# Kernel tuning notes

Measured on AMD Instinct MI355X. Metric: run time of the kernel, lower is better.

## Reference

```python
import jax, jax.numpy as jnp
import numpy as np

NUM_LAYERS = 3


def setup_inputs() -> dict:
    key = jax.random.key(0)
    k1, k2 = jax.random.split(key)
    N = 200000          # num_users + num_items
    D = 64              # latent_dim
    E = 4000000         # number of directed edges
    edge_index = jax.random.randint(k1, (2, E), 0, N, dtype=jnp.int64)
    emb_weight = 0.1 * jax.random.normal(k2, (N, D), dtype=jnp.float32)  # nn.init.normal_(std=0.1)
    return {"edge_index": edge_index, "emb_weight": emb_weight}


def reference(edge_index, emb_weight):
    N, D = emb_weight.shape
    src, dst = edge_index[0], edge_index[1]
    # gcn_norm (no self loops), as used by LGConv
    deg = jax.ops.segment_sum(jnp.ones_like(src, dtype=emb_weight.dtype), dst, num_segments=N)
    dinv = jnp.where(deg > 0, jax.lax.rsqrt(jnp.maximum(deg, 1.0)), 0.0)
    norm = dinv[src] * dinv[dst]            # [E]
    emb0 = emb_weight
    emb = emb0
    acc = emb0                              # running sum over layer embeddings
    for _ in range(NUM_LAYERS):
        msgs = norm[:, None] * emb[src]     # [E, D] irregular gather
        emb = jax.ops.segment_sum(msgs, dst, num_segments=N)  # scatter-add aggregate
        acc = acc + emb
    out = acc / (NUM_LAYERS + 1)            # mean over stacked layer embeddings
    return (emb0, out)
```

## Files before the change

### kernel.cpp

```cpp
#include <hip/hip_runtime.h>

#define DIM 64
#define BNODE_SHIFT 9
#define BNODE (1 << BNODE_SHIFT)
#define MAXNB 512
#define BIN_CHUNK 8192

__device__ inline float bf2f(unsigned short h) {
    return __uint_as_float(((unsigned int)h) << 16);
}
__device__ inline unsigned int f2bf2(float a, float b) {
    unsigned int ua = __float_as_uint(a);
    unsigned int ub = __float_as_uint(b);
    ua = (ua + 0x7FFFu + ((ua >> 16) & 1u)) >> 16;
    ub = (ub + 0x7FFFu + ((ub >> 16) & 1u)) >> 16;
    return ua | (ub << 16);
}

__global__ void hist_kernel(const int* __restrict__ dst, int* __restrict__ bucket_count,
                            int E, int NB) {
    __shared__ int h[MAXNB];
    const int t = threadIdx.x;
    for (int i = t; i < MAXNB; i += blockDim.x) h[i] = 0;
    __syncthreads();
    const long long beg = (long long)blockIdx.x * BIN_CHUNK;
    for (int j = 0; j < BIN_CHUNK / 256; ++j) {
        long long idx = beg + j * 256 + t;
        if (idx < E) atomicAdd(&h[dst[idx] >> BNODE_SHIFT], 1);
    }
    __syncthreads();
    for (int b = t; b < NB; b += blockDim.x)
        if (h[b]) atomicAdd(&bucket_count[b], h[b]);
}

__global__ void __launch_bounds__(MAXNB) bucket_scan_kernel(
        const int* __restrict__ bucket_count, int* __restrict__ bucket_base,
        int* __restrict__ bucket_cursor, int* __restrict__ row_start,
        int NB, int N, int E) {
    __shared__ int s[MAXNB];
    const int t = threadIdx.x;
    int c = (t < NB) ? bucket_count[t] : 0;
    s[t] = c;
    __syncthreads();
    for (int off = 1; off < MAXNB; off <<= 1) {
        int v = s[t];
        int a = (t >= off) ? s[t - off] : 0;
        __syncthreads();
        s[t] = v + a;
        __syncthreads();
    }
    if (t < NB) {
        int excl = s[t] - c;
        bucket_base[t] = excl;
        bucket_cursor[t] = excl;
    }
    if (t == 0) {
        bucket_base[NB] = s[MAXNB - 1];
        row_start[N] = E;
    }
}

__global__ void bin_kernel(const int* __restrict__ src, const int* __restrict__ dst,
                           int* __restrict__ bucket_cursor, unsigned int* __restrict__ packed,
                           int E, int NB) {
    __shared__ int lhist[MAXNB];
    __shared__ int lbase[MAXNB];
    const int t = threadIdx.x;
    for (int i = t; i < MAXNB; i += blockDim.x) lhist[i] = 0;
    __syncthreads();
    const long long beg = (long long)blockIdx.x * BIN_CHUNK;
    for (int j = 0; j < BIN_CHUNK / 256; ++j) {
        long long idx = beg + j * 256 + t;
        if (idx < E) atomicAdd(&lhist[dst[idx] >> BNODE_SHIFT], 1);
    }
    __syncthreads();
    for (int b = t; b < NB; b += blockDim.x) {
        int c = lhist[b];
        lbase[b] = c ? atomicAdd(&bucket_cursor[b], c) : 0;
    }
    __syncthreads();
    for (int i = t; i < MAXNB; i += blockDim.x) lhist[i] = 0;
    __syncthreads();
    for (int j = 0; j < BIN_CHUNK / 256; ++j) {
        long long idx = beg + j * 256 + t;
        if (idx < E) {
            int d = dst[idx];
            int b = d >> BNODE_SHIFT;
            int lpos = atomicAdd(&lhist[b], 1);
            packed[lbase[b] + lpos] =
                (unsigned int)src[idx] | ((unsigned int)(d & (BNODE - 1)) << 18);
        }
    }
}

__global__ void __launch_bounds__(BNODE) csr_kernel(
        const int* __restrict__ bucket_base, const unsigned int* __restrict__ packed,
        int* __restrict__ csr_src, int* __restrict__ row_start,
        float* __restrict__ dinv, float* __restrict__ rs, float* __restrict__ di2,
        int N) {
    __shared__ int hist[BNODE];
    __shared__ int s[BNODE];
    const int t = threadIdx.x;
    const int b = blockIdx.x;
    const int b0 = bucket_base[b];
    const int cnt = bucket_base[b + 1] - b0;
    hist[t] = 0;
    __syncthreads();
    for (int i = t; i < cnt; i += BNODE)
        atomicAdd(&hist[packed[b0 + i] >> 18], 1);
    __syncthreads();
    s[t] = hist[t];
    __syncthreads();
    for (int off = 1; off < BNODE; off <<= 1) {
        int v = s[t];
        int a = (t >= off) ? s[t - off] : 0;
        __syncthreads();
        s[t] = v + a;
        __syncthreads();
    }
    const int deg = hist[t];
    const int excl = s[t] - deg;
    const int node = (b << BNODE_SHIFT) + t;
    if (node < N) {
        row_start[node] = b0 + excl;
        float fd = (float)deg;
        float di = deg > 0 ? rsqrtf(fd) : 0.0f;
        dinv[node] = di;
        rs[node]   = deg > 0 ? sqrtf(fd) : 0.0f;
        di2[node]  = di * di;
    }
    __syncthreads();
    s[t] = excl;
    __syncthreads();
    for (int i = t; i < cnt; i += BNODE) {
        unsigned int p = packed[b0 + i];
        int lpos = atomicAdd(&s[p >> 18], 1);
        csr_src[b0 + lpos] = (int)(p & 0x3FFFFu);
    }
}

__global__ void conv0_kernel(const float* __restrict__ emb0, const float* __restrict__ dinv,
                             float* __restrict__ out_emb0, unsigned int* __restrict__ S0,
                             int n4) {
    int i = blockIdx.x * blockDim.x + threadIdx.x;
    if (i >= n4) return;
    float4 v = ((const float4*)emb0)[i];
    ((float4*)out_emb0)[i] = v;
    float w = dinv[i >> 4];
    uint2 o;
    o.x = f2bf2(w * v.x, w * v.y);
    o.y = f2bf2(w * v.z, w * v.w);
    ((uint2*)S0)[i] = o;
}

__global__ void gather_kernel(const int* __restrict__ row_start,
                              const int* __restrict__ csr_src,
                              const float* __restrict__ di2,
                              const unsigned int* __restrict__ S_in,
                              unsigned int* __restrict__ S_out,
                              int N) {
    int tid = blockIdx.x * blockDim.x + threadIdx.x;
    int node = tid >> 3;
    int q = tid & 7;
    if (node >= N) return;
    const int beg = row_start[node];
    const int end = row_start[node + 1];
    float r0 = 0.f, r1 = 0.f, r2 = 0.f, r3 = 0.f, r4 = 0.f, r5 = 0.f, r6 = 0.f, r7 = 0.f;
    for (int i = beg; i < end; ++i) {
        int sIdx = csr_src[i];
        uint4 g = *(const uint4*)(S_in + (size_t)sIdx * (DIM / 2) + q * 4);
        r0 += bf2f((unsigned short)(g.x & 0xFFFF));
        r1 += bf2f((unsigned short)(g.x >> 16));
        r2 += bf2f((unsigned short)(g.y & 0xFFFF));
        r3 += bf2f((unsigned short)(g.y >> 16));
        r4 += bf2f((unsigned short)(g.z & 0xFFFF));
        r5 += bf2f((unsigned short)(g.z >> 16));
        r6 += bf2f((unsigned short)(g.w & 0xFFFF));
        r7 += bf2f((unsigned short)(g.w >> 16));
    }
    float w = di2[node];
    uint4 o;
    o.x = f2bf2(w * r0, w * r1);
    o.y = f2bf2(w * r2, w * r3);
    o.z = f2bf2(w * r4, w * r5);
    o.w = f2bf2(w * r6, w * r7);
    *(uint4*)(S_out + (size_t)node * (DIM / 2) + q * 4) = o;
}

__global__ void combine_kernel(const float* __restrict__ emb0, const float* __restrict__ rs,
                               const unsigned int* __restrict__ S1,
                               const unsigned int* __restrict__ S2,
                               const unsigned int* __restrict__ S3,
                               float* __restrict__ acc, int n4) {
    int i = blockIdx.x * blockDim.x + threadIdx.x;
    if (i >= n4) return;
    float4 e = ((const float4*)emb0)[i];
    uint2 a = ((const uint2*)S1)[i];
    uint2 b = ((const uint2*)S2)[i];
    uint2 c = ((const uint2*)S3)[i];
    float w = rs[i >> 4];
    float4 o;
    o.x = 0.25f * (e.x + w * (bf2f(a.x & 0xFFFF) + bf2f(b.x & 0xFFFF) + bf2f(c.x & 0xFFFF)));
    o.y = 0.25f * (e.y + w * (bf2f(a.x >> 16)   + bf2f(b.x >> 16)   + bf2f(c.x >> 16)));
    o.z = 0.25f * (e.z + w * (bf2f(a.y & 0xFFFF) + bf2f(b.y & 0xFFFF) + bf2f(c.y & 0xFFFF)));
    o.w = 0.25f * (e.w + w * (bf2f(a.y >> 16)   + bf2f(b.y >> 16)   + bf2f(c.y >> 16)));
    ((float4*)acc)[i] = o;
}

static inline size_t align256(size_t x) { return (x + 255) & ~(size_t)255; }

extern "C" void kernel_launch(void* const* d_in, const int* in_sizes, int n_in,
                              void* d_out, int out_size, void* d_ws, size_t ws_size,
                              hipStream_t stream) {
    const int*   edge = (const int*)d_in[0];
    const float* emb0 = (const float*)d_in[1];
    const int E = in_sizes[0] / 2;
    const int N = in_sizes[1] / DIM;
    const int* src = edge;
    const int* dst = edge + E;
    const int NB = (N + BNODE - 1) >> BNODE_SHIFT;

    char* ws = (char*)d_ws;
    int* bucket_count  = (int*)ws;  ws += align256((size_t)(MAXNB + 1) * sizeof(int));
    int* bucket_base   = (int*)ws;  ws += align256((size_t)(MAXNB + 1) * sizeof(int));
    int* bucket_cursor = (int*)ws;  ws += align256((size_t)(MAXNB + 1) * sizeof(int));
    int* row_start     = (int*)ws;  ws += align256((size_t)(N + 1) * sizeof(int));
    float* dinv        = (float*)ws; ws += align256((size_t)N * sizeof(float));
    float* rs          = (float*)ws; ws += align256((size_t)N * sizeof(float));
    float* di2         = (float*)ws; ws += align256((size_t)N * sizeof(float));
    unsigned int* packed  = (unsigned int*)ws; ws += align256((size_t)E * sizeof(int));
    int* csr_src       = (int*)ws;  ws += align256((size_t)E * sizeof(int));
    unsigned int* SX   = (unsigned int*)ws; ws += align256((size_t)N * DIM / 2 * sizeof(unsigned int) / 2 * 2 + 256);
    unsigned int* SY   = (unsigned int*)ws; ws += align256((size_t)N * (DIM / 2) * sizeof(unsigned int));
    unsigned int* SZ   = (unsigned int*)ws; ws += align256((size_t)N * (DIM / 2) * sizeof(unsigned int));

    float* out_emb0 = (float*)d_out;
    float* acc      = out_emb0 + (size_t)N * DIM;

    const int blocks_e = (int)(((long long)E + BIN_CHUNK - 1) / BIN_CHUNK);
    const int n4 = N * DIM / 4;

    hipMemsetAsync(bucket_count, 0, (size_t)(MAXNB + 1) * sizeof(int), stream);
    hist_kernel<<<blocks_e, 256, 0, stream>>>(dst, bucket_count, E, NB);
    bucket_scan_kernel<<<1, MAXNB, 0, stream>>>(bucket_count, bucket_base, bucket_cursor,
                                                row_start, NB, N, E);
    bin_kernel<<<blocks_e, 256, 0, stream>>>(src, dst, bucket_cursor, packed, E, NB);
    csr_kernel<<<NB, BNODE, 0, stream>>>(bucket_base, packed, csr_src, row_start,
                                         dinv, rs, di2, N);

    conv0_kernel<<<(n4 + 255) / 256, 256, 0, stream>>>(emb0, dinv, out_emb0, SX, n4);

    const int gthreads = N * 8;
    const int ggrid = (gthreads + 255) / 256;
    gather_kernel<<<ggrid, 256, 0, stream>>>(row_start, csr_src, di2, SX, SY, N);
    gather_kernel<<<ggrid, 256, 0, stream>>>(row_start, csr_src, di2, SY, SX, N);
    gather_kernel<<<ggrid, 256, 0, stream>>>(row_start, csr_src, di2, SX, SZ, N);

    combine_kernel<<<(n4 + 255) / 256, 256, 0, stream>>>(emb0, rs, SY, SX, SZ, acc, n4);
}
```

Measured before the change: 585.6 us.

## Degree-sort nodes per bucket and fuse combine into final gather layer

The CSR kernel now counting-sorts the nodes within each 512-node bucket by degree and emits a per-node descriptor (row begin, row end, node id, 1/deg). The gather kernels walk these descriptors so that neighbouring wavefront lanes handle nodes of similar degree, which is meant to cut loop divergence. The final gather layer folds in the combine step, reading emb0 and the two earlier layer buffers and writing acc directly, which removes a separate pass and the third intermediate buffer. In exchange, the output writes become scattered because nodes are permuted, the CSR kernel gains an extra scan, and the weights are now derived from 1/deg through sqrt and rsqrt.

Measured after the change: 608.1 us. 1.04x slower.

```diff
diff --git a/kernel.cpp b/kernel.cpp
--- a/kernel.cpp
+++ b/kernel.cpp
@@ -6,8 +6,8 @@
 #define MAXNB 512
 #define BIN_CHUNK 8192
 
-__device__ inline float bf2f(unsigned short h) {
-    return __uint_as_float(((unsigned int)h) << 16);
+__device__ inline float bf2f(unsigned int h) {
+    return __uint_as_float((h & 0xFFFFu) << 16);
 }
 __device__ inline unsigned int f2bf2(float a, float b) {
     unsigned int ua = __float_as_uint(a);
@@ -35,8 +35,7 @@
 
 __global__ void __launch_bounds__(MAXNB) bucket_scan_kernel(
         const int* __restrict__ bucket_count, int* __restrict__ bucket_base,
-        int* __restrict__ bucket_cursor, int* __restrict__ row_start,
-        int NB, int N, int E) {
+        int* __restrict__ bucket_cursor, int NB) {
     __shared__ int s[MAXNB];
     const int t = threadIdx.x;
     int c = (t < NB) ? bucket_count[t] : 0;
@@ -54,10 +53,7 @@
         bucket_base[t] = excl;
         bucket_cursor[t] = excl;
     }
-    if (t == 0) {
-        bucket_base[NB] = s[MAXNB - 1];
-        row_start[N] = E;
-    }
+    if (t == 0) bucket_base[NB] = s[MAXNB - 1];
 }
 
 __global__ void bin_kernel(const int* __restrict__ src, const int* __restrict__ dst,
@@ -95,9 +91,8 @@
 
 __global__ void __launch_bounds__(BNODE) csr_kernel(
         const int* __restrict__ bucket_base, const unsigned int* __restrict__ packed,
-        int* __restrict__ csr_src, int* __restrict__ row_start,
-        float* __restrict__ dinv, float* __restrict__ rs, float* __restrict__ di2,
-        int N) {
+        int* __restrict__ csr_src, float* __restrict__ dinv,
+        int4* __restrict__ desc, int N) {
     __shared__ int hist[BNODE];
     __shared__ int s[BNODE];
     const int t = threadIdx.x;
@@ -120,14 +115,13 @@
     }
     const int deg = hist[t];
     const int excl = s[t] - deg;
+    const int myBeg = b0 + excl;
     const int node = (b << BNODE_SHIFT) + t;
+    float di2 = 0.0f;
     if (node < N) {
-        row_start[node] = b0 + excl;
         float fd = (float)deg;
-        float di = deg > 0 ? rsqrtf(fd) : 0.0f;
-        dinv[node] = di;
-        rs[node]   = deg > 0 ? sqrtf(fd) : 0.0f;
-        di2[node]  = di * di;
+        di2 = deg > 0 ? 1.0f / fd : 0.0f;
+        dinv[node] = deg > 0 ? rsqrtf(fd) : 0.0f;
     }
     __syncthreads();
     s[t] = excl;
@@ -137,6 +131,28 @@
         int lpos = atomicAdd(&s[p >> 18], 1);
         csr_src[b0 + lpos] = (int)(p & 0x3FFFFu);
     }
+    __syncthreads();
+    const int bin = deg < (BNODE - 1) ? deg : (BNODE - 1);
+    hist[t] = 0;
+    __syncthreads();
+    atomicAdd(&hist[bin], 1);
+    __syncthreads();
+    s[t] = hist[t];
+    __syncthreads();
+    for (int off = 1; off < BNODE; off <<= 1) {
+        int v = s[t];
+        int a = (t >= off) ? s[t - off] : 0;
+        __syncthreads();
+        s[t] = v + a;
+        __syncthreads();
+    }
+    int tot = hist[t];
+    __syncthreads();
+    hist[t] = s[t] - tot;
+    __syncthreads();
+    int pos = atomicAdd(&hist[bin], 1);
+    desc[(b << BNODE_SHIFT) + pos] =
+        make_int4(myBeg, myBeg + deg, node < N ? node : 0x7FFFFFFF, __float_as_int(di2));
 }
 
 __global__ void conv0_kernel(const float* __restrict__ emb0, const float* __restrict__ dinv,
@@ -153,58 +169,64 @@
     ((uint2*)S0)[i] = o;
 }
 
-__global__ void gather_kernel(const int* __restrict__ row_start,
+template<bool LAST>
+__global__ void gather_kernel(const int4* __restrict__ desc,
                               const int* __restrict__ csr_src,
-                              const float* __restrict__ di2,
                               const unsigned int* __restrict__ S_in,
                               unsigned int* __restrict__ S_out,
-                              int N) {
+                              const unsigned int* __restrict__ S1,
+                              const float* __restrict__ emb0,
+                              float* __restrict__ acc,
+                              int N, int NG) {
     int tid = blockIdx.x * blockDim.x + threadIdx.x;
-    int node = tid >> 3;
+    int g = tid >> 3;
     int q = tid & 7;
+    if (g >= NG) return;
+    const int4 d = desc[g];
+    const int node = d.z;
     if (node >= N) return;
-    const int beg = row_start[node];
-    const int end = row_start[node + 1];
     float r0 = 0.f, r1 = 0.f, r2 = 0.f, r3 = 0.f, r4 = 0.f, r5 = 0.f, r6 = 0.f, r7 = 0.f;
-    for (int i = beg; i < end; ++i) {
+    for (int i = d.x; i < d.y; ++i) {
         int sIdx = csr_src[i];
-        uint4 g = *(const uint4*)(S_in + (size_t)sIdx * (DIM / 2) + q * 4);
-        r0 += bf2f((unsigned short)(g.x & 0xFFFF));
-        r1 += bf2f((unsigned short)(g.x >> 16));
-        r2 += bf2f((unsigned short)(g.y & 0xFFFF));
-        r3 += bf2f((unsigned short)(g.y >> 16));
-        r4 += bf2f((unsigned short)(g.z & 0xFFFF));
-        r5 += bf2f((unsigned short)(g.z >> 16));
-        r6 += bf2f((unsigned short)(g.w & 0xFFFF));
-        r7 += bf2f((unsigned short)(g.w >> 16));
-    }
-    float w = di2[node];
-    uint4 o;
-    o.x = f2bf2(w * r0, w * r1);
-    o.y = f2bf2(w * r2, w * r3);
-    o.z = f2bf2(w * r4, w * r5);
-    o.w = f2bf2(w * r6, w * r7);
-    *(uint4*)(S_out + (size_t)node * (DIM / 2) + q * 4) = o;
-}
-
-__global__ void combine_kernel(const float* __restrict__ emb0, const float* __restrict__ rs,
-                               const unsigned int* __restrict__ S1,
-                               const unsigned int* __restrict__ S2,
-                               const unsigned int* __restrict__ S3,
-                               float* __restrict__ acc, int n4) {
-    int i = blockIdx.x * blockDim.x + threadIdx.x;
-    if (i >= n4) return;
-    float4 e = ((const float4*)emb0)[i];
-    uint2 a = ((const uint2*)S1)[i];
-    uint2 b = ((const uint2*)S2)[i];
-    uint2 c = ((const uint2*)S3)[i];
-    float w = rs[i >> 4];
-    float4 o;
-    o.x = 0.25f * (e.x + w * (bf2f(a.x & 0xFFFF) + bf2f(b.x & 0xFFFF) + bf2f(c.x & 0xFFFF)));
-    o.y = 0.25f * (e.y + w * (bf2f(a.x >> 16)   + bf2f(b.x >> 16)   + bf2f(c.x >> 16)));
-    o.z = 0.25f * (e.z + w * (bf2f(a.y & 0xFFFF) + bf2f(b.y & 0xFFFF) + bf2f(c.y & 0xFFFF)));
-    o.w = 0.25f * (e.w + w * (bf2f(a.y >> 16)   + bf2f(b.y >> 16)   + bf2f(c.y >> 16)));
-    ((float4*)acc)[i] = o;
+        uint4 gg = *(const uint4*)(S_in + (size_t)sIdx * (DIM / 2) + q * 4);
+        r0 += bf2f(gg.x);
+        r1 += bf2f(gg.x >> 16);
+        r2 += bf2f(gg.y);
+        r3 += bf2f(gg.y >> 16);
+        r4 += bf2f(gg.z);
+        r5 += bf2f(gg.z >> 16);
+        r6 += bf2f(gg.w);
+        r7 += bf2f(gg.w >> 16);
+    }
+    const float di2 = __int_as_float(d.w);
+    if (!LAST) {
+        uint4 o;
+        o.x = f2bf2(di2 * r0, di2 * r1);
+        o.y = f2bf2(di2 * r2, di2 * r3);
+        o.z = f2bf2(di2 * r4, di2 * r5);
+        o.w = f2bf2(di2 * r6, di2 * r7);
+        *(uint4*)(S_out + (size_t)node * (DIM / 2) + q * 4) = o;
+    } else {
+        float rs = di2 > 0.f ? rsqrtf(di2) : 0.f;
+        float dv = sqrtf(di2);
+        uint4 a1 = *(const uint4*)(S1   + (size_t)node * (DIM / 2) + q * 4);
+        uint4 a2 = *(const uint4*)(S_in + (size_t)node * (DIM / 2) + q * 4);
+        const float* e = emb0 + (size_t)node * DIM + q * 8;
+        float4 e0 = *(const float4*)(e);
+        float4 e1 = *(const float4*)(e + 4);
+        float4 o0, o1;
+        o0.x = 0.25f * (e0.x + rs * (bf2f(a1.x) + bf2f(a2.x)) + dv * r0);
+        o0.y = 0.25f * (e0.y + rs * (bf2f(a1.x >> 16) + bf2f(a2.x >> 16)) + dv * r1);
+        o0.z = 0.25f * (e0.z + rs * (bf2f(a1.y) + bf2f(a2.y)) + dv * r2);
+        o0.w = 0.25f * (e0.w + rs * (bf2f(a1.y >> 16) + bf2f(a2.y >> 16)) + dv * r3);
+        o1.x = 0.25f * (e1.x + rs * (bf2f(a1.z) + bf2f(a2.z)) + dv * r4);
+        o1.y = 0.25f * (e1.y + rs * (bf2f(a1.z >> 16) + bf2f(a2.z >> 16)) + dv * r5);
+        o1.z = 0.25f * (e1.z + rs * (bf2f(a1.w) + bf2f(a2.w)) + dv * r6);
+        o1.w = 0.25f * (e1.w + rs * (bf2f(a1.w >> 16) + bf2f(a2.w >> 16)) + dv * r7);
+        float* ap = acc + (size_t)node * DIM + q * 8;
+        *(float4*)(ap) = o0;
+        *(float4*)(ap + 4) = o1;
+    }
 }
 
 static inline size_t align256(size_t x) { return (x + 255) & ~(size_t)255; }
@@ -224,15 +246,12 @@
     int* bucket_count  = (int*)ws;  ws += align256((size_t)(MAXNB + 1) * sizeof(int));
     int* bucket_base   = (int*)ws;  ws += align256((size_t)(MAXNB + 1) * sizeof(int));
     int* bucket_cursor = (int*)ws;  ws += align256((size_t)(MAXNB + 1) * sizeof(int));
-    int* row_start     = (int*)ws;  ws += align256((size_t)(N + 1) * sizeof(int));
     float* dinv        = (float*)ws; ws += align256((size_t)N * sizeof(float));
-    float* rs          = (float*)ws; ws += align256((size_t)N * sizeof(float));
-    float* di2         = (float*)ws; ws += align256((size_t)N * sizeof(float));
-    unsigned int* packed  = (unsigned int*)ws; ws += align256((size_t)E * sizeof(int));
+    int4* desc         = (int4*)ws; ws += align256((size_t)NB * BNODE * sizeof(int4));
+    unsigned int* packed = (unsigned int*)ws; ws += align256((size_t)E * sizeof(int));
     int* csr_src       = (int*)ws;  ws += align256((size_t)E * sizeof(int));
-    unsigned int* SX   = (unsigned int*)ws; ws += align256((size_t)N * DIM / 2 * sizeof(unsigned int) / 2 * 2 + 256);
+    unsigned int* SX   = (unsigned int*)ws; ws += align256((size_t)N * (DIM / 2) * sizeof(unsigned int));
     unsigned int* SY   = (unsigned int*)ws; ws += align256((size_t)N * (DIM / 2) * sizeof(unsigned int));
-    unsigned int* SZ   = (unsigned int*)ws; ws += align256((size_t)N * (DIM / 2) * sizeof(unsigned int));
 
     float* out_emb0 = (float*)d_out;
     float* acc      = out_emb0 + (size_t)N * DIM;
@@ -242,19 +261,15 @@
 
     hipMemsetAsync(bucket_count, 0, (size_t)(MAXNB + 1) * sizeof(int), stream);
     hist_kernel<<<blocks_e, 256, 0, stream>>>(dst, bucket_count, E, NB);
-    bucket_scan_kernel<<<1, MAXNB, 0, stream>>>(bucket_count, bucket_base, bucket_cursor,
-                                                row_start, NB, N, E);
+    bucket_scan_kernel<<<1, MAXNB, 0, stream>>>(bucket_count, bucket_base, bucket_cursor, NB);
     bin_kernel<<<blocks_e, 256, 0, stream>>>(src, dst, bucket_cursor, packed, E, NB);
-    csr_kernel<<<NB, BNODE, 0, stream>>>(bucket_base, packed, csr_src, row_start,
-                                         dinv, rs, di2, N);
+    csr_kernel<<<NB, BNODE, 0, stream>>>(bucket_base, packed, csr_src, dinv, desc, N);
 
     conv0_kernel<<<(n4 + 255) / 256, 256, 0, stream>>>(emb0, dinv, out_emb0, SX, n4);
 
-    const int gthreads = N * 8;
-    const int ggrid = (gthreads + 255) / 256;
-    gather_kernel<<<ggrid, 256, 0, stream>>>(row_start, csr_src, di2, SX, SY, N);
-    gather_kernel<<<ggrid, 256, 0, stream>>>(row_start, csr_src, di2, SY, SX, N);
-    gather_kernel<<<ggrid, 256, 0, stream>>>(row_start, csr_src, di2, SX, SZ, N);
-
-    combine_kernel<<<(n4 + 255) / 256, 256, 0, stream>>>(emb0, rs, SY, SX, SZ, acc, n4);
-}
+    const int NG = NB * BNODE;
+    const int ggrid = (NG * 8 + 255) / 256;
+    gather_kernel<false><<<ggrid, 256, 0, stream>>>(desc, csr_src, SX, SY, nullptr, nullptr, nullptr, N, NG);
+    gather_kernel<false><<<ggrid, 256, 0, stream>>>(desc, csr_src, SY, SX, nullptr, nullptr, nullptr, N, NG);
+    gather_kernel<true><<<ggrid, 256, 0, stream>>>(desc, csr_src, SX, nullptr, SY, emb0, acc, N, NG);
+}
```
